# Kernel tuning notes

Measured on AMD Instinct MI355X. Metric: run time of the kernel, lower is better.

Reference implementation:

```python
import jax, jax.numpy as jnp
import numpy as np

RES = jnp.array([2.0, 2.0, 2.0], dtype=jnp.float32)  # voxel spacing (mm) for x,y,z step distances


def setup_inputs() -> dict:
    key = jax.random.key(0)
    k1, k2 = jax.random.split(key)
    B, H, D, W = 4, 128, 512, 512
    G, P = 72, 65536
    ct_stack = jax.random.normal(k1, (B, H, D, W), dtype=jnp.float32)
    # coords are (x, y, z) voxel-space floats; clamp ranges in forward are (W-1, D-1, H-1)
    scale = jnp.array([W - 1, D - 1, H - 1], dtype=jnp.float32)
    stacked_indices = jax.random.uniform(k2, (1, G, P, 3), dtype=jnp.float32) * scale
    return {"ct_stack": ct_stack, "stacked_indices": stacked_indices}


def reference(ct_stack, stacked_indices):
    B, H, D, W = ct_stack.shape
    _, G, P, _ = stacked_indices.shape
    c = stacked_indices[0]  # [G,P,3]; identical for every batch element (buffer expand)
    x = jnp.clip(c[..., 0], 0, W - 1)
    y = jnp.clip(c[..., 1], 0, D - 1)
    z = jnp.clip(c[..., 2], 0, H - 1)
    x0 = jnp.floor(x).astype(jnp.int32)
    y0 = jnp.floor(y).astype(jnp.int32)
    z0 = jnp.floor(z).astype(jnp.int32)
    x1 = jnp.clip(x0 + 1, 0, W - 1)
    y1 = jnp.clip(y0 + 1, 0, D - 1)
    z1 = jnp.clip(z0 + 1, 0, H - 1)
    xd = x - x0.astype(x.dtype)
    yd = y - y0.astype(y.dtype)
    zd = z - z0.astype(z.dtype)

    ct_flat = ct_stack.reshape(B, H * D * W)
    lin = lambda zz, yy, xx: (zz * D + yy) * W + xx  # linear index into flattened [H,D,W]
    g = lambda idx: jnp.take(ct_flat, idx, axis=1)   # [B,G,P]

    c000 = g(lin(z0, y0, x0)); c001 = g(lin(z0, y0, x1))
    c010 = g(lin(z0, y1, x0)); c011 = g(lin(z0, y1, x1))
    c100 = g(lin(z1, y0, x0)); c101 = g(lin(z1, y0, x1))
    c110 = g(lin(z1, y1, x0)); c111 = g(lin(z1, y1, x1))

    c00 = c000 * (1 - xd) + c001 * xd
    c01 = c010 * (1 - xd) + c011 * xd
    c10 = c100 * (1 - xd) + c101 * xd
    c11 = c110 * (1 - xd) + c111 * xd
    c0 = c00 * (1 - yd) + c01 * yd
    c1 = c10 * (1 - yd) + c11 * yd
    density = c0 * (1 - zd) + c1 * zd  # [B,G,P]

    # per-angle mean physical step size along the sampled line
    diff = c[:, 1:, :] - c[:, :-1, :]          # [G,P-1,3]
    physical_diff = diff * RES
    step_distances = jnp.sqrt(jnp.sum(physical_diff ** 2, axis=-1))  # [G,P-1]
    step_sizes = jnp.mean(step_distances, axis=-1).reshape(1, G, 1)

    cumsum = jnp.cumsum(density, axis=-1) * step_sizes
    cumsum = cumsum + density * step_sizes * 0.5
    return cumsum.reshape(B * G, P, 1)
```

## Files before the change

### kernel.cpp

```cpp
#include <hip/hip_runtime.h>
#include <math.h>

#define BB 4
#define HH 128
#define DD 512
#define WW 512
#define GG 72
#define PP 65536
#define CHUNK 256
#define NCHUNK (PP / CHUNK)
#define HDW (HH * DD * WW)
#define NBRICK (HDW / 8)
#define CPB 2
#define NPART (NCHUNK / CPB)

typedef _Float16 half4 __attribute__((ext_vector_type(4)));
typedef _Float16 half8 __attribute__((ext_vector_type(8)));
typedef float f4 __attribute__((ext_vector_type(4)));

__global__ __launch_bounds__(256) void k_transpose(
    const float* __restrict__ ct, _Float16* __restrict__ tv)
{
    const int n2  = blockIdx.x * 256 + threadIdx.x;
    const int bxp = n2 & 127;
    const int by  = (n2 >> 7) & 255;
    const int bz  = n2 >> 15;
    const size_t base = ((size_t)(2 * bz) * DD + 2 * by) * WW + 4 * bxp;

    half8 o00, o01, o02, o03;
    half8 o10, o11, o12, o13;
#pragma unroll
    for (int b = 0; b < BB; ++b) {
        const float* v = ct + (size_t)b * HDW + base;
        const f4 f00 = __builtin_nontemporal_load((const f4*)(v));
        const f4 f01 = __builtin_nontemporal_load((const f4*)(v + WW));
        const f4 f10 = __builtin_nontemporal_load((const f4*)(v + (size_t)DD * WW));
        const f4 f11 = __builtin_nontemporal_load((const f4*)(v + (size_t)DD * WW + WW));
        o00[b] = (_Float16)f00[0]; o00[4 + b] = (_Float16)f00[1];
        o01[b] = (_Float16)f01[0]; o01[4 + b] = (_Float16)f01[1];
        o02[b] = (_Float16)f10[0]; o02[4 + b] = (_Float16)f10[1];
        o03[b] = (_Float16)f11[0]; o03[4 + b] = (_Float16)f11[1];
        o10[b] = (_Float16)f00[2]; o10[4 + b] = (_Float16)f00[3];
        o11[b] = (_Float16)f01[2]; o11[4 + b] = (_Float16)f01[3];
        o12[b] = (_Float16)f10[2]; o12[4 + b] = (_Float16)f10[3];
        o13[b] = (_Float16)f11[2]; o13[4 + b] = (_Float16)f11[3];
    }
    _Float16* dst = tv + (size_t)n2 * 64;
    *(half8*)(dst)      = o00;
    *(half8*)(dst + 8)  = o01;
    *(half8*)(dst + 16) = o02;
    *(half8*)(dst + 24) = o03;
    *(half8*)(dst + 32) = o10;
    *(half8*)(dst + 40) = o11;
    *(half8*)(dst + 48) = o12;
    *(half8*)(dst + 56) = o13;
}

__device__ __forceinline__ int brick_off(int zc, int yc, int xc)
{
    const int brick = ((zc >> 1) << 16) | ((yc >> 1) << 8) | (xc >> 1);
    const int inner = ((zc & 1) << 2) | ((yc & 1) << 1) | (xc & 1);
    return (brick << 5) | (inner << 2);
}

struct PS {
    int i[8];
    float xd, yd, zd;
};

__device__ __forceinline__ PS setup_brick(float cx, float cy, float cz)
{
    const float x = fminf(fmaxf(cx, 0.0f), (float)(WW - 1));
    const float y = fminf(fmaxf(cy, 0.0f), (float)(DD - 1));
    const float z = fminf(fmaxf(cz, 0.0f), (float)(HH - 1));
    const int x0 = (int)floorf(x);
    const int y0 = (int)floorf(y);
    const int z0 = (int)floorf(z);
    const int x1 = min(x0 + 1, WW - 1);
    const int y1 = min(y0 + 1, DD - 1);
    const int z1 = min(z0 + 1, HH - 1);
    PS s;
    s.xd = x - (float)x0;
    s.yd = y - (float)y0;
    s.zd = z - (float)z0;
    s.i[0] = brick_off(z0, y0, x0); s.i[1] = brick_off(z0, y0, x1);
    s.i[2] = brick_off(z0, y1, x0); s.i[3] = brick_off(z0, y1, x1);
    s.i[4] = brick_off(z1, y0, x0); s.i[5] = brick_off(z1, y0, x1);
    s.i[6] = brick_off(z1, y1, x0); s.i[7] = brick_off(z1, y1, x1);
    return s;
}

__device__ __forceinline__ void gather8(
    const _Float16* __restrict__ tv, const PS& s, half4 A[8])
{
#pragma unroll
    for (int k = 0; k < 8; ++k) A[k] = *(const half4*)(tv + (size_t)s.i[k]);
}

__device__ __forceinline__ void lerp_store(
    const half4 A[8], const PS& s, float dens[BB],
    float* __restrict__ density, int g, int p)
{
#pragma unroll
    for (int b = 0; b < BB; ++b) {
        const float c000 = (float)A[0][b], c001 = (float)A[1][b];
        const float c010 = (float)A[2][b], c011 = (float)A[3][b];
        const float c100 = (float)A[4][b], c101 = (float)A[5][b];
        const float c110 = (float)A[6][b], c111 = (float)A[7][b];
        const float c00 = c000 * (1.0f - s.xd) + c001 * s.xd;
        const float c01 = c010 * (1.0f - s.xd) + c011 * s.xd;
        const float c10 = c100 * (1.0f - s.xd) + c101 * s.xd;
        const float c11 = c110 * (1.0f - s.xd) + c111 * s.xd;
        const float c0  = c00 * (1.0f - s.yd) + c01 * s.yd;
        const float c1  = c10 * (1.0f - s.yd) + c11 * s.yd;
        dens[b] = c0 * (1.0f - s.zd) + c1 * s.zd;
        __builtin_nontemporal_store(dens[b],
            density + ((size_t)(b * GG + g)) * PP + p);
    }
}

__global__ __launch_bounds__(256) void k_density_h(
    const _Float16* __restrict__ tv,
    const float* __restrict__ coords,
    float* __restrict__ density,
    float* __restrict__ chunk_sums,
    float* __restrict__ dist_part)
{
    const int cpair = blockIdx.x;
    const int g     = blockIdx.y;
    const int t     = threadIdx.x;
    const int c0    = cpair * CPB;
    const int p0    = c0 * CHUNK + t;

    __shared__ float cbuf[(CPB * CHUNK + 1) * 3];
    const bool last  = (cpair == NPART - 1);
    const int  nload = last ? CPB * CHUNK * 3 : (CPB * CHUNK + 1) * 3;
    const float* src = coords + ((size_t)g * PP + (size_t)c0 * CHUNK) * 3;
    for (int i = t; i < nload; i += 256)
        cbuf[i] = __builtin_nontemporal_load(src + i);
    __syncthreads();

    const float ax = cbuf[3 * t + 0], ay = cbuf[3 * t + 1], az = cbuf[3 * t + 2];
    const int   u  = t + 256;
    const float bx = cbuf[3 * u + 0], by = cbuf[3 * u + 1], bz = cbuf[3 * u + 2];

    float dist_tot;
    {
        const float dx = cbuf[3 * (t + 1) + 0] - ax;
        const float dy = cbuf[3 * (t + 1) + 1] - ay;
        const float dz = cbuf[3 * (t + 1) + 2] - az;
        dist_tot = sqrtf(dx * dx + dy * dy + dz * dz);
    }
    if (!(last && t == CHUNK - 1)) {
        const float dx = cbuf[3 * (u + 1) + 0] - bx;
        const float dy = cbuf[3 * (u + 1) + 1] - by;
        const float dz = cbuf[3 * (u + 1) + 2] - bz;
        dist_tot += sqrtf(dx * dx + dy * dy + dz * dz);
    }

    const PS s0 = setup_brick(ax, ay, az);
    const PS s1 = setup_brick(bx, by, bz);

    half4 A0[8], A1[8];
    gather8(tv, s0, A0);
    gather8(tv, s1, A1);

    float dens0[BB], dens1[BB];
    lerp_store(A0, s0, dens0, density, g, p0);
    lerp_store(A1, s1, dens1, density, g, p0 + 256);

    __shared__ float wsum[4][9];
    const int lane = t & 63;
    const int wid  = t >> 6;
    float r[9] = {dens0[0], dens0[1], dens0[2], dens0[3],
                  dens1[0], dens1[1], dens1[2], dens1[3], dist_tot};
#pragma unroll
    for (int off = 32; off > 0; off >>= 1) {
#pragma unroll
        for (int k = 0; k < 9; ++k) r[k] += __shfl_xor(r[k], off);
    }
    if (lane == 0) {
#pragma unroll
        for (int k = 0; k < 9; ++k) wsum[wid][k] = r[k];
    }
    __syncthreads();
    if (t == 0) {
        float sarr[9];
#pragma unroll
        for (int k = 0; k < 9; ++k)
            sarr[k] = wsum[0][k] + wsum[1][k] + wsum[2][k] + wsum[3][k];
#pragma unroll
        for (int b = 0; b < BB; ++b) {
            chunk_sums[((size_t)(b * GG + g)) * NCHUNK + c0]     = sarr[b];
            chunk_sums[((size_t)(b * GG + g)) * NCHUNK + c0 + 1] = sarr[4 + b];
        }
        dist_part[g * NPART + cpair] = sarr[8];
    }
}

__global__ __launch_bounds__(256) void k_density(
    const float* __restrict__ ct,
    const float* __restrict__ coords,
    float* __restrict__ density,
    float* __restrict__ chunk_sums,
    float* __restrict__ dist_part)
{
    const int chunk = blockIdx.x;
    const int g     = blockIdx.y;
    const int t     = threadIdx.x;
    const int p     = chunk * CHUNK + t;

    __shared__ float cbuf[(CHUNK + 1) * 3];
    const int nload = (chunk == NCHUNK - 1) ? CHUNK * 3 : (CHUNK + 1) * 3;
    const float* src = coords + ((size_t)g * PP + (size_t)chunk * CHUNK) * 3;
    for (int i = t; i < nload; i += CHUNK) cbuf[i] = src[i];
    __syncthreads();

    const float cx = cbuf[3 * t + 0];
    const float cy = cbuf[3 * t + 1];
    const float cz = cbuf[3 * t + 2];

    float dist = 0.0f;
    if (p < PP - 1) {
        const int nt = 3 * (t + 1);
        const float dx = cbuf[nt + 0] - cx;
        const float dy = cbuf[nt + 1] - cy;
        const float dz = cbuf[nt + 2] - cz;
        dist = sqrtf(dx * dx + dy * dy + dz * dz);
    }

    const float x = fminf(fmaxf(cx, 0.0f), (float)(WW - 1));
    const float y = fminf(fmaxf(cy, 0.0f), (float)(DD - 1));
    const float z = fminf(fmaxf(cz, 0.0f), (float)(HH - 1));
    const int x0 = (int)floorf(x);
    const int y0 = (int)floorf(y);
    const int z0 = (int)floorf(z);
    const int x1 = min(x0 + 1, WW - 1);
    const int y1 = min(y0 + 1, DD - 1);
    const int z1 = min(z0 + 1, HH - 1);
    const float xd = x - (float)x0, yd = y - (float)y0, zd = z - (float)z0;

    const int b00 = (z0 * DD + y0) * WW;
    const int b01 = (z0 * DD + y1) * WW;
    const int b10 = (z1 * DD + y0) * WW;
    const int b11 = (z1 * DD + y1) * WW;

    float dens[BB];
#pragma unroll
    for (int b = 0; b < BB; ++b) {
        const float* v = ct + (size_t)b * HDW;
        const float c000 = v[b00 + x0], c001 = v[b00 + x1];
        const float c010 = v[b01 + x0], c011 = v[b01 + x1];
        const float c100 = v[b10 + x0], c101 = v[b10 + x1];
        const float c110 = v[b11 + x0], c111 = v[b11 + x1];
        const float c00 = c000 * (1.0f - xd) + c001 * xd;
        const float c01 = c010 * (1.0f - xd) + c011 * xd;
        const float c10 = c100 * (1.0f - xd) + c101 * xd;
        const float c11 = c110 * (1.0f - xd) + c111 * xd;
        const float c0  = c00 * (1.0f - yd) + c01 * yd;
        const float c1  = c10 * (1.0f - yd) + c11 * yd;
        dens[b] = c0 * (1.0f - zd) + c1 * zd;
        density[((size_t)(b * GG + g)) * PP + p] = dens[b];
    }

    __shared__ float wsum[4][5];
    const int lane = t & 63;
    const int wid  = t >> 6;
    float r0 = dens[0], r1 = dens[1], r2 = dens[2], r3 = dens[3], rd = dist;
#pragma unroll
    for (int off = 32; off > 0; off >>= 1) {
        r0 += __shfl_xor(r0, off);
        r1 += __shfl_xor(r1, off);
        r2 += __shfl_xor(r2, off);
        r3 += __shfl_xor(r3, off);
        rd += __shfl_xor(rd, off);
    }
    if (lane == 0) {
        wsum[wid][0] = r0; wsum[wid][1] = r1; wsum[wid][2] = r2;
        wsum[wid][3] = r3; wsum[wid][4] = rd;
    }
    __syncthreads();
    if (t == 0) {
        float s0 = 0, s1 = 0, s2 = 0, s3 = 0, sd = 0;
#pragma unroll
        for (int w = 0; w < 4; ++w) {
            s0 += wsum[w][0]; s1 += wsum[w][1]; s2 += wsum[w][2];
            s3 += wsum[w][3]; sd += wsum[w][4];
        }
        chunk_sums[((size_t)(0 * GG + g)) * NCHUNK + chunk] = s0;
        chunk_sums[((size_t)(1 * GG + g)) * NCHUNK + chunk] = s1;
        chunk_sums[((size_t)(2 * GG + g)) * NCHUNK + chunk] = s2;
        chunk_sums[((size_t)(3 * GG + g)) * NCHUNK + chunk] = s3;
        dist_part[g * NCHUNK + chunk] = sd;
    }
}

__global__ __launch_bounds__(256) void k_output(
    float* __restrict__ out,
    const float* __restrict__ cs,
    const float* __restrict__ dist_part,
    int npart)
{
    const int chunk = blockIdx.x;
    const int g     = blockIdx.y;
    const int t     = threadIdx.x;
    const int p     = chunk * CHUNK + t;
    const int lane  = t & 63;
    const int wid   = t >> 6;

    float d[BB], v[BB];
#pragma unroll
    for (int b = 0; b < BB; ++b)
        d[b] = __builtin_nontemporal_load(out + ((size_t)(b * GG + g)) * PP + p);

    __shared__ float exl[4];
    __shared__ float sdist;

    {
        const float* row = cs + ((size_t)(wid * GG + g)) * NCHUNK;
        float pv = 0.0f;
#pragma unroll
        for (int k = 0; k < 4; ++k) {
            const int idx = lane + 64 * k;
            const float x = row[idx];
            pv += (idx < chunk) ? x : 0.0f;
        }
#pragma unroll
        for (int off = 32; off > 0; off >>= 1) pv += __shfl_xor(pv, off);
        if (lane == 0) exl[wid] = pv;
    }
    if (wid == 0) {
        float dv = 0.0f;
#pragma unroll
        for (int k = 0; k < 4; ++k) {
            const int idx = lane + 64 * k;
            dv += (idx < npart) ? dist_part[g * npart + idx] : 0.0f;
        }
#pragma unroll
        for (int off = 32; off > 0; off >>= 1) dv += __shfl_xor(dv, off);
        if (lane == 0) sdist = dv;
    }

#pragma unroll
    for (int b = 0; b < BB; ++b) v[b] = d[b];

#pragma unroll
    for (int dd = 1; dd < 64; dd <<= 1) {
#pragma unroll
        for (int b = 0; b < BB; ++b) {
            const float n = __shfl_up(v[b], dd);
            if (lane >= dd) v[b] += n;
        }
    }
    __shared__ float ws[4][BB];
    if (lane == 63) {
#pragma unroll
        for (int b = 0; b < BB; ++b) ws[wid][b] = v[b];
    }
    __syncthreads();

    const float step = sdist * (2.0f / (float)(PP - 1));
#pragma unroll
    for (int b = 0; b < BB; ++b) {
        float prefix = 0.0f;
        for (int w = 0; w < wid; ++w) prefix += ws[w][b];
        const float excl = exl[b];
        const float incl = excl + prefix + v[b];
        __builtin_nontemporal_store(step * (incl + 0.5f * d[b]),
            out + ((size_t)(b * GG + g)) * PP + p);
    }
}

extern "C" void kernel_launch(void* const* d_in, const int* in_sizes, int n_in,
                              void* d_out, int out_size, void* d_ws, size_t ws_size,
                              hipStream_t stream)
{
    const float* ct     = (const float*)d_in[0];
    const float* coords = (const float*)d_in[1];
    float* out = (float*)d_out;

    const size_t volBytes = (size_t)HDW * BB * sizeof(_Float16);
    const size_t csCount  = (size_t)BB * GG * NCHUNK;
    const size_t dpCount  = (size_t)GG * NCHUNK;
    const size_t needed   = volBytes + (csCount + dpCount) * sizeof(float);

    if (ws_size >= needed) {
        _Float16* tv       = (_Float16*)d_ws;
        float* chunk_sums  = (float*)((char*)d_ws + volBytes);
        float* dist_part   = chunk_sums + csCount;

        k_transpose<<<NBRICK / 2 / 256, 256, 0, stream>>>(ct, tv);
        k_density_h<<<dim3(NCHUNK / CPB, GG), 256, 0, stream>>>(tv, coords, out, chunk_sums, dist_part);
        k_output<<<dim3(NCHUNK, GG), 256, 0, stream>>>(out, chunk_sums, dist_part, NPART);
    } else {
        float* chunk_sums  = (float*)d_ws;
        float* dist_part   = chunk_sums + csCount;

        k_density<<<dim3(NCHUNK, GG), 256, 0, stream>>>(ct, coords, out, chunk_sums, dist_part);
        k_output<<<dim3(NCHUNK, GG), 256, 0, stream>>>(out, chunk_sums, dist_part, NCHUNK);
    }
}
```

Measured before the change: 1.008 ms.

## Move intra-chunk prefix scan into density kernels, recover density by differencing

The density kernels now run the within-chunk inclusive scan (wave shuffle-up plus a cross-wave prefix) and store chunk-local prefix sums instead of raw densities. The output kernel drops its own scan and recovers each point's density as the difference between neighbouring prefixes, taking the value across a wave boundary from shared memory. The scan work is done while gather results are already in registers, which shortens the output pass. The trade-off is a small loss of precision from subtracting prefixes, plus an occupancy hint of 8 blocks per CU and interleaved gather issue in the half-precision kernel.

```diff
diff --git a/kernel.cpp b/kernel.cpp
--- a/kernel.cpp
+++ b/kernel.cpp
@@ -97,9 +97,8 @@
     for (int k = 0; k < 8; ++k) A[k] = *(const half4*)(tv + (size_t)s.i[k]);
 }
 
-__device__ __forceinline__ void lerp_store(
-    const half4 A[8], const PS& s, float dens[BB],
-    float* __restrict__ density, int g, int p)
+__device__ __forceinline__ void lerp8(
+    const half4 A[8], float xd, float yd, float zd, float dens[BB])
 {
 #pragma unroll
     for (int b = 0; b < BB; ++b) {
@@ -107,19 +106,17 @@
         const float c010 = (float)A[2][b], c011 = (float)A[3][b];
         const float c100 = (float)A[4][b], c101 = (float)A[5][b];
         const float c110 = (float)A[6][b], c111 = (float)A[7][b];
-        const float c00 = c000 * (1.0f - s.xd) + c001 * s.xd;
-        const float c01 = c010 * (1.0f - s.xd) + c011 * s.xd;
-        const float c10 = c100 * (1.0f - s.xd) + c101 * s.xd;
-        const float c11 = c110 * (1.0f - s.xd) + c111 * s.xd;
-        const float c0  = c00 * (1.0f - s.yd) + c01 * s.yd;
-        const float c1  = c10 * (1.0f - s.yd) + c11 * s.yd;
-        dens[b] = c0 * (1.0f - s.zd) + c1 * s.zd;
-        __builtin_nontemporal_store(dens[b],
-            density + ((size_t)(b * GG + g)) * PP + p);
-    }
-}
-
-__global__ __launch_bounds__(256) void k_density_h(
+        const float c00 = c000 * (1.0f - xd) + c001 * xd;
+        const float c01 = c010 * (1.0f - xd) + c011 * xd;
+        const float c10 = c100 * (1.0f - xd) + c101 * xd;
+        const float c11 = c110 * (1.0f - xd) + c111 * xd;
+        const float c0  = c00 * (1.0f - yd) + c01 * yd;
+        const float c1  = c10 * (1.0f - yd) + c11 * yd;
+        dens[b] = c0 * (1.0f - zd) + c1 * zd;
+    }
+}
+
+__global__ __launch_bounds__(256, 8) void k_density_h(
     const _Float16* __restrict__ tv,
     const float* __restrict__ coords,
     float* __restrict__ density,
@@ -158,43 +155,58 @@
         dist_tot += sqrtf(dx * dx + dy * dy + dz * dz);
     }
 
+    half4 A0[8], A1[8];
     const PS s0 = setup_brick(ax, ay, az);
+    gather8(tv, s0, A0);
     const PS s1 = setup_brick(bx, by, bz);
-
-    half4 A0[8], A1[8];
-    gather8(tv, s0, A0);
     gather8(tv, s1, A1);
 
-    float dens0[BB], dens1[BB];
-    lerp_store(A0, s0, dens0, density, g, p0);
-    lerp_store(A1, s1, dens1, density, g, p0 + 256);
-
-    __shared__ float wsum[4][9];
+    float v0[BB], v1[BB];
+    lerp8(A0, s0.xd, s0.yd, s0.zd, v0);
+    lerp8(A1, s1.xd, s1.yd, s1.zd, v1);
+
     const int lane = t & 63;
     const int wid  = t >> 6;
-    float r[9] = {dens0[0], dens0[1], dens0[2], dens0[3],
-                  dens1[0], dens1[1], dens1[2], dens1[3], dist_tot};
-#pragma unroll
-    for (int off = 32; off > 0; off >>= 1) {
-#pragma unroll
-        for (int k = 0; k < 9; ++k) r[k] += __shfl_xor(r[k], off);
-    }
-    if (lane == 0) {
-#pragma unroll
-        for (int k = 0; k < 9; ++k) wsum[wid][k] = r[k];
-    }
+#pragma unroll
+    for (int d = 1; d < 64; d <<= 1) {
+#pragma unroll
+        for (int b = 0; b < BB; ++b) {
+            const float n0 = __shfl_up(v0[b], d);
+            const float n1 = __shfl_up(v1[b], d);
+            if (lane >= d) { v0[b] += n0; v1[b] += n1; }
+        }
+    }
+    float rd = dist_tot;
+#pragma unroll
+    for (int off = 32; off > 0; off >>= 1) rd += __shfl_xor(rd, off);
+
+    __shared__ float wtot[4][9];
+    if (lane == 63) {
+#pragma unroll
+        for (int b = 0; b < BB; ++b) { wtot[wid][b] = v0[b]; wtot[wid][4 + b] = v1[b]; }
+    }
+    if (lane == 0) wtot[wid][8] = rd;
     __syncthreads();
+
+#pragma unroll
+    for (int b = 0; b < BB; ++b) {
+        float pre0 = 0.0f, pre1 = 0.0f;
+        for (int w = 0; w < wid; ++w) { pre0 += wtot[w][b]; pre1 += wtot[w][4 + b]; }
+        __builtin_nontemporal_store(v0[b] + pre0,
+            density + ((size_t)(b * GG + g)) * PP + p0);
+        __builtin_nontemporal_store(v1[b] + pre1,
+            density + ((size_t)(b * GG + g)) * PP + p0 + 256);
+    }
+
     if (t == 0) {
-        float sarr[9];
-#pragma unroll
-        for (int k = 0; k < 9; ++k)
-            sarr[k] = wsum[0][k] + wsum[1][k] + wsum[2][k] + wsum[3][k];
 #pragma unroll
         for (int b = 0; b < BB; ++b) {
-            chunk_sums[((size_t)(b * GG + g)) * NCHUNK + c0]     = sarr[b];
-            chunk_sums[((size_t)(b * GG + g)) * NCHUNK + c0 + 1] = sarr[4 + b];
+            chunk_sums[((size_t)(b * GG + g)) * NCHUNK + c0] =
+                wtot[0][b] + wtot[1][b] + wtot[2][b] + wtot[3][b];
+            chunk_sums[((size_t)(b * GG + g)) * NCHUNK + c0 + 1] =
+                wtot[0][4 + b] + wtot[1][4 + b] + wtot[2][4 + b] + wtot[3][4 + b];
         }
-        dist_part[g * NPART + cpair] = sarr[8];
+        dist_part[g * NPART + cpair] = wtot[0][8] + wtot[1][8] + wtot[2][8] + wtot[3][8];
     }
 }
 
@@ -245,53 +257,58 @@
     const int b10 = (z1 * DD + y0) * WW;
     const int b11 = (z1 * DD + y1) * WW;
 
-    float dens[BB];
-#pragma unroll
-    for (int b = 0; b < BB; ++b) {
-        const float* v = ct + (size_t)b * HDW;
-        const float c000 = v[b00 + x0], c001 = v[b00 + x1];
-        const float c010 = v[b01 + x0], c011 = v[b01 + x1];
-        const float c100 = v[b10 + x0], c101 = v[b10 + x1];
-        const float c110 = v[b11 + x0], c111 = v[b11 + x1];
+    float v[BB];
+#pragma unroll
+    for (int b = 0; b < BB; ++b) {
+        const float* vp = ct + (size_t)b * HDW;
+        const float c000 = vp[b00 + x0], c001 = vp[b00 + x1];
+        const float c010 = vp[b01 + x0], c011 = vp[b01 + x1];
+        const float c100 = vp[b10 + x0], c101 = vp[b10 + x1];
+        const float c110 = vp[b11 + x0], c111 = vp[b11 + x1];
         const float c00 = c000 * (1.0f - xd) + c001 * xd;
         const float c01 = c010 * (1.0f - xd) + c011 * xd;
         const float c10 = c100 * (1.0f - xd) + c101 * xd;
         const float c11 = c110 * (1.0f - xd) + c111 * xd;
         const float c0  = c00 * (1.0f - yd) + c01 * yd;
         const float c1  = c10 * (1.0f - yd) + c11 * yd;
-        dens[b] = c0 * (1.0f - zd) + c1 * zd;
-        density[((size_t)(b * GG + g)) * PP + p] = dens[b];
-    }
-
-    __shared__ float wsum[4][5];
+        v[b] = c0 * (1.0f - zd) + c1 * zd;
+    }
+
     const int lane = t & 63;
     const int wid  = t >> 6;
-    float r0 = dens[0], r1 = dens[1], r2 = dens[2], r3 = dens[3], rd = dist;
-#pragma unroll
-    for (int off = 32; off > 0; off >>= 1) {
-        r0 += __shfl_xor(r0, off);
-        r1 += __shfl_xor(r1, off);
-        r2 += __shfl_xor(r2, off);
-        r3 += __shfl_xor(r3, off);
-        rd += __shfl_xor(rd, off);
-    }
-    if (lane == 0) {
-        wsum[wid][0] = r0; wsum[wid][1] = r1; wsum[wid][2] = r2;
-        wsum[wid][3] = r3; wsum[wid][4] = rd;
-    }
+#pragma unroll
+    for (int d = 1; d < 64; d <<= 1) {
+#pragma unroll
+        for (int b = 0; b < BB; ++b) {
+            const float n = __shfl_up(v[b], d);
+            if (lane >= d) v[b] += n;
+        }
+    }
+    float rd = dist;
+#pragma unroll
+    for (int off = 32; off > 0; off >>= 1) rd += __shfl_xor(rd, off);
+
+    __shared__ float wtot[4][5];
+    if (lane == 63) {
+#pragma unroll
+        for (int b = 0; b < BB; ++b) wtot[wid][b] = v[b];
+    }
+    if (lane == 0) wtot[wid][4] = rd;
     __syncthreads();
+
+#pragma unroll
+    for (int b = 0; b < BB; ++b) {
+        float pre = 0.0f;
+        for (int w = 0; w < wid; ++w) pre += wtot[w][b];
+        density[((size_t)(b * GG + g)) * PP + p] = v[b] + pre;
+    }
     if (t == 0) {
-        float s0 = 0, s1 = 0, s2 = 0, s3 = 0, sd = 0;
-#pragma unroll
-        for (int w = 0; w < 4; ++w) {
-            s0 += wsum[w][0]; s1 += wsum[w][1]; s2 += wsum[w][2];
-            s3 += wsum[w][3]; sd += wsum[w][4];
-        }
-        chunk_sums[((size_t)(0 * GG + g)) * NCHUNK + chunk] = s0;
-        chunk_sums[((size_t)(1 * GG + g)) * NCHUNK + chunk] = s1;
-        chunk_sums[((size_t)(2 * GG + g)) * NCHUNK + chunk] = s2;
-        chunk_sums[((size_t)(3 * GG + g)) * NCHUNK + chunk] = s3;
-        dist_part[g * NCHUNK + chunk] = sd;
+#pragma unroll
+        for (int b = 0; b < BB; ++b)
+            chunk_sums[((size_t)(b * GG + g)) * NCHUNK + chunk] =
+                wtot[0][b] + wtot[1][b] + wtot[2][b] + wtot[3][b];
+        dist_part[g * NCHUNK + chunk] =
+            wtot[0][4] + wtot[1][4] + wtot[2][4] + wtot[3][4];
     }
 }
 
@@ -308,13 +325,14 @@
     const int lane  = t & 63;
     const int wid   = t >> 6;
 
-    float d[BB], v[BB];
+    float v[BB];
 #pragma unroll
     for (int b = 0; b < BB; ++b)
-        d[b] = __builtin_nontemporal_load(out + ((size_t)(b * GG + g)) * PP + p);
+        v[b] = __builtin_nontemporal_load(out + ((size_t)(b * GG + g)) * PP + p);
 
     __shared__ float exl[4];
     __shared__ float sdist;
+    __shared__ float edge[4][BB];
 
     {
         const float* row = cs + ((size_t)(wid * GG + g)) * NCHUNK;
@@ -341,32 +359,19 @@
         if (lane == 0) sdist = dv;
     }
 
-#pragma unroll
-    for (int b = 0; b < BB; ++b) v[b] = d[b];
-
-#pragma unroll
-    for (int dd = 1; dd < 64; dd <<= 1) {
-#pragma unroll
-        for (int b = 0; b < BB; ++b) {
-            const float n = __shfl_up(v[b], dd);
-            if (lane >= dd) v[b] += n;
-        }
-    }
-    __shared__ float ws[4][BB];
     if (lane == 63) {
 #pragma unroll
-        for (int b = 0; b < BB; ++b) ws[wid][b] = v[b];
+        for (int b = 0; b < BB; ++b) edge[wid][b] = v[b];
     }
     __syncthreads();
 
     const float step = sdist * (2.0f / (float)(PP - 1));
 #pragma unroll
     for (int b = 0; b < BB; ++b) {
-        float prefix = 0.0f;
-        for (int w = 0; w < wid; ++w) prefix += ws[w][b];
-        const float excl = exl[b];
-        const float incl = excl + prefix + v[b];
-        __builtin_nontemporal_store(step * (incl + 0.5f * d[b]),
+        const float n    = __shfl_up(v[b], 1);
+        const float prev = (lane > 0) ? n : (wid > 0 ? edge[wid - 1][b] : 0.0f);
+        const float d    = v[b] - prev;
+        __builtin_nontemporal_store(step * (exl[b] + v[b] + 0.5f * d),
             out + ((size_t)(b * GG + g)) * PP + p);
     }
 }
```

After: 1.060 ms. +5.1%, slower.
